# Kernel tuning notes

Measured on AMD Instinct MI355X. Metric: run time of the kernel, lower is better.

Reference implementation:

```python
import jax, jax.numpy as jnp
import numpy as np

EPS = 1e-5
V = 16  # num_nodes

def _bn(x, g, b, axes, ch):
    # training-mode BatchNorm (biased variance), channel axis = ch
    m = x.mean(axes, keepdims=True)
    v = x.var(axes, keepdims=True)
    sh = [1] * x.ndim
    sh[ch] = x.shape[ch]
    return (x - m) * jax.lax.rsqrt(v + EPS) * g.reshape(sh) + b.reshape(sh)

def _adp(nv1, nv2, max_num_neigh=1):
    # softmax(relu(nv1 @ nv2), dim=1), then keep entries > max(1/V, (k+1)-th largest) with straight-through mask
    A = jax.nn.softmax(jax.nn.relu(nv1 @ nv2), axis=1)
    kth = -jnp.sort(-A, axis=1)[:, max_num_neigh:max_num_neigh + 1]  # (k+1)-th largest per row == -kthvalue(-A, k+1)
    mask = ((A > 1.0 / A.shape[0]) & (A > kth)).astype(A.dtype)
    binm = jax.lax.stop_gradient(mask - A) + A  # straight-through estimator
    return A * binm

def _stgcn(x, A, gw, gb, b1g, b1b, tw, tb, b2g, b2b):
    # standard ST-GCN block with spatial kernel K=1, stride 1, identity residual (in==out)
    # x: (N,C,T,V)
    res = x
    y = jnp.einsum('oc,nctv->notv', gw, x) + gb[None, :, None, None]  # 1x1 conv
    y = jnp.einsum('nctv,vw->nctw', y, A)                              # graph aggregation
    y = jax.nn.relu(_bn(y, b1g, b1b, (0, 2, 3), 1))
    y = jax.lax.conv_general_dilated(y, tw[:, :, :, None], (1, 1), [(1, 1), (0, 0)],
                                     dimension_numbers=('NCHW', 'OIHW', 'NCHW'))  # temporal conv (kt,1)
    y = _bn(y + tb[None, :, None, None], b2g, b2b, (0, 2, 3), 1)
    return jax.nn.relu(y + res)

def _static(x, pw, pg, pb, tw, tg, tb):
    # x: (p,n,c,s)
    p, n, c, s = x.shape
    # p-branch: Conv1d(c->c, k=1, no bias) over node dim + BN1d (stats over n*s batch and length p)
    y = jnp.einsum('oc,pncs->nsop', pw, x)          # (n,s,c,p)
    y = _bn(y, pg, pb, (0, 1, 3), 2)
    # t-branch: grouped Conv1d over time, groups = p nodes, kernel 3, pad 1
    z = y.transpose(0, 3, 2, 1).reshape(n, p * c, s)
    z = jax.lax.conv_general_dilated(z, tw, (1,), [(1, 1)],
                                     dimension_numbers=('NCH', 'OIH', 'NCH'),
                                     feature_group_count=p)
    z = _bn(z, tg, tb, (0, 2), 1)
    return z.reshape(n, p, c, s).transpose(1, 0, 2, 3)  # (p,n,c,s)

def _forward(x, nv1, nv2,
             d1gw, d1gb, d1b1g, d1b1b, d1tw, d1tb, d1b2g, d1b2b,
             d2gw, d2gb, d2b1g, d2b1b, d2tw, d2tb, d2b2g, d2b2b,
             s1pw, s1pg, s1pb, s1tw, s1tg, s1tb,
             s2pw, s2pg, s2pb, s2tw, s2tg, s2tb):
    A = _adp(nv1, nv2, 1)
    d = _stgcn(x, A, d1gw, d1gb, d1b1g, d1b1b, d1tw, d1tb, d1b2g, d1b2b)
    d = _stgcn(d, A, d2gw, d2gb, d2b1g, d2b1b, d2tw, d2tb, d2b2g, d2b2b)
    d = d.max(axis=2)                      # (N,C,V) max over time
    xs = x.transpose(3, 0, 1, 2)           # (V,N,C,T)
    s = _static(xs, s1pw, s1pg, s1pb, s1tw, s1tg, s1tb)
    s = _static(s, s2pw, s2pg, s2pb, s2tw, s2tg, s2tb)
    s = s.transpose(1, 2, 3, 0).max(axis=2)  # (N,C,V)
    return jnp.concatenate([d, s], axis=2)   # (N,C,2V)

def setup_inputs():
    key = jax.random.key(0)
    N, C, T, kt = 32, 128, 256, 3
    ks = jax.random.split(key, 8)
    def nrm(k, sh, s=0.05):
        return jax.random.normal(k, sh, jnp.float32) * s
    inp = {'x': nrm(ks[0], (N, C, T, V), 1.0),
           'nv1': nrm(ks[1], (V, 64), 1.0),
           'nv2': nrm(ks[2], (64, V), 1.0)}
    def stgcn_p(k, pre):
        k1, k2 = jax.random.split(k)
        return {pre + 'gw': nrm(k1, (C, C)), pre + 'gb': jnp.zeros(C),
                pre + 'b1g': jnp.ones(C), pre + 'b1b': jnp.zeros(C),
                pre + 'tw': nrm(k2, (C, C, kt)), pre + 'tb': jnp.zeros(C),
                pre + 'b2g': jnp.ones(C), pre + 'b2b': jnp.zeros(C)}
    def static_p(k, pre):
        k1, k2 = jax.random.split(k)
        return {pre + 'pw': nrm(k1, (C, C)), pre + 'pg': jnp.ones(C), pre + 'pb': jnp.zeros(C),
                pre + 'tw': nrm(k2, (V * C, C, kt)), pre + 'tg': jnp.ones(V * C), pre + 'tb': jnp.zeros(V * C)}
    inp.update(stgcn_p(ks[3], 'd1'))
    inp.update(stgcn_p(ks[4], 'd2'))
    inp.update(static_p(ks[5], 's1'))
    inp.update(static_p(ks[6], 's2'))
    return inp

def reference(x, nv1, nv2,
              d1gw, d1gb, d1b1g, d1b1b, d1tw, d1tb, d1b2g, d1b2b,
              d2gw, d2gb, d2b1g, d2b1b, d2tw, d2tb, d2b2g, d2b2b,
              s1pw, s1pg, s1pb, s1tw, s1tg, s1tb,
              s2pw, s2pg, s2pb, s2tw, s2tg, s2tb):
    return _forward(x, nv1, nv2,
                    d1gw, d1gb, d1b1g, d1b1b, d1tw, d1tb, d1b2g, d1b2b,
                    d2gw, d2gb, d2b1g, d2b1b, d2tw, d2tb, d2b2g, d2b2b,
                    s1pw, s1pg, s1pb, s1tw, s1tg, s1tb,
                    s2pw, s2pg, s2pb, s2tw, s2tg, s2tb)
```

## Files before the change

### kernel.cpp

```cpp
#include <hip/hip_runtime.h>

#define EPSBN 1e-5f

typedef __attribute__((ext_vector_type(8))) __bf16 bf16x8;
typedef __attribute__((ext_vector_type(4))) float f32x4;
typedef __attribute__((ext_vector_type(8))) unsigned short us8;

__device__ inline unsigned short f2bf(float f) {
  unsigned u = __float_as_uint(f);
  u = (u + 0x7fffu + ((u >> 16) & 1u)) >> 16;
  return (unsigned short)u;
}
__device__ inline float bf2f(unsigned short h) {
  return __uint_as_float(((unsigned)h) << 16);
}

__global__ void k_adj(const float* __restrict__ nv1, const float* __restrict__ nv2,
                      float* __restrict__ A, float* __restrict__ sA,
                      int* __restrict__ cntA, int* __restrict__ lvA, float* __restrict__ lvalA) {
  __shared__ float M[16][16];
  int tid = threadIdx.x;
  int i = tid >> 4, j = tid & 15;
  float acc = 0.f;
  #pragma unroll
  for (int k = 0; k < 64; ++k) acc += nv1[i*64+k] * nv2[k*16+j];
  M[i][j] = fmaxf(acc, 0.f);
  __syncthreads();
  if (tid < 16) {
    float m = -1e30f;
    for (int c = 0; c < 16; ++c) m = fmaxf(m, M[tid][c]);
    float e[16]; float s = 0.f;
    for (int c = 0; c < 16; ++c) { e[c] = expf(M[tid][c] - m); s += e[c]; }
    float inv = 1.f / s;
    float t1 = -1e30f, t2 = -1e30f;
    for (int c = 0; c < 16; ++c) {
      float a = e[c] * inv; e[c] = a;
      if (a > t1) { t2 = t1; t1 = a; }
      else if (a > t2) t2 = a;
    }
    for (int c = 0; c < 16; ++c) {
      bool keep = (e[c] > (1.0f/16.0f)) && (e[c] > t2);
      M[tid][c] = keep ? e[c] : 0.f;
    }
  }
  __syncthreads();
  A[tid] = M[tid>>4][tid&15];
  if (tid < 16) {
    float s = 0.f;
    int cnt = 0;
    for (int v = 0; v < 16; ++v) {
      float a = M[v][tid];
      s += a;
      if (a != 0.f) { lvA[tid*16 + cnt] = v; lvalA[tid*16 + cnt] = a; ++cnt; }
    }
    sA[tid] = s;
    cntA[tid] = cnt;
  }
}

__global__ __launch_bounds__(256) void k_cvt_cw(const float* __restrict__ w,
                                                unsigned short* __restrict__ o) {
  int idx = blockIdx.x*256 + threadIdx.x;
  if (idx < 16384) o[idx] = f2bf(w[idx]);
}
__global__ __launch_bounds__(256) void k_cvt_tw(const float* __restrict__ w,
                                                unsigned short* __restrict__ o, int nOut) {
  int idx = blockIdx.x*256 + threadIdx.x;
  if (idx >= nOut*384) return;
  int oo = idx / 384;
  int r = idx - oo*384;
  int tap = r >> 7, c = r & 127;
  o[idx] = f2bf(w[(oo*128 + c)*3 + tap]);
}

__global__ __launch_bounds__(256) void k_xS(const float* __restrict__ x,
                                            unsigned short* __restrict__ xS) {
  __shared__ float tl[64*128];
  int b = blockIdx.x; int n = b >> 6; int t0q = b & 63;
  int tid = threadIdx.x;
  const float* xb = x + (long)n*524288 + t0q*64;
  for (int idx = tid; idx < 2048; idx += 256) {
    int c = idx >> 4, q = idx & 15;
    float4 v = *(const float4*)(xb + (long)c*4096 + q*4);
    int cb = c >> 2, cl = c & 3;
    #pragma unroll
    for (int j = 0; j < 4; ++j)
      tl[(4*q+j)*128 + (((cb ^ q) & 31) << 2) + cl] = ((const float*)&v)[j];
  }
  __syncthreads();
  for (int idx = tid; idx < 2048; idx += 256) {
    int pos = idx >> 5, cblk = idx & 31;
    f32x4 v = *(const f32x4*)&tl[pos*128 + (((cblk ^ (pos >> 2)) & 31) << 2)];
    ushort4 pk;
    pk.x = f2bf(v.x); pk.y = f2bf(v.y); pk.z = f2bf(v.z); pk.w = f2bf(v.w);
    int vv = pos & 15, tt = pos >> 4;
    *(ushort4*)(xS + ((long)(n*16+vv)*256 + t0q*4 + tt)*128 + cblk*4) = pk;
  }
}

__global__ __launch_bounds__(256) void k_aggGconv(
    const float* __restrict__ x,
    const int* __restrict__ cntA, const int* __restrict__ lvA, const float* __restrict__ lvalA,
    const unsigned short* __restrict__ Wb,
    unsigned short* __restrict__ out,
    const float* __restrict__ gb, const float* __restrict__ sAv,
    float* __restrict__ part)
{
  __shared__ float tl[64*128];
  __shared__ __align__(16) unsigned short Th[64*128];
  __shared__ int cntS[16];
  __shared__ int lvS[256];
  __shared__ float lvalS[256];
  int b = blockIdx.x; int n = b >> 6; int off = (b & 63) << 6;
  int tid = threadIdx.x;
  if (tid < 16) cntS[tid] = cntA[tid];
  lvS[tid] = lvA[tid];
  lvalS[tid] = lvalA[tid];
  const float* xb = x + (long)n*524288 + off;
  for (int idx = tid; idx < 2048; idx += 256) {
    int c = idx >> 4, q = idx & 15;
    float4 v = *(const float4*)(xb + (long)c*4096 + q*4);
    int cb = c >> 2, cl = c & 3;
    #pragma unroll
    for (int j = 0; j < 4; ++j)
      tl[(4*q+j)*128 + (((cb ^ q) & 31) << 2) + cl] = ((const float*)&v)[j];
  }
  __syncthreads();
  for (int idx = tid; idx < 1024; idx += 256) {
    int pos = idx >> 4, c8 = (idx & 15) << 3;
    int tt = pos >> 4, w = pos & 15;
    int cb0 = c8 >> 2, cb1 = cb0 + 1;
    f32x4 s0 = {0.f,0.f,0.f,0.f}, s1 = {0.f,0.f,0.f,0.f};
    int cw = cntS[w];
    for (int j = 0; j < cw; ++j) {
      int p = tt*16 + lvS[w*16 + j];
      float a = lvalS[w*16 + j];
      int sw = p >> 2;
      f32x4 x0 = *(const f32x4*)&tl[p*128 + (((cb0 ^ sw) & 31) << 2)];
      f32x4 x1 = *(const f32x4*)&tl[p*128 + (((cb1 ^ sw) & 31) << 2)];
      s0.x += a*x0.x; s0.y += a*x0.y; s0.z += a*x0.z; s0.w += a*x0.w;
      s1.x += a*x1.x; s1.y += a*x1.y; s1.z += a*x1.z; s1.w += a*x1.w;
    }
    us8 pk;
    pk[0]=f2bf(s0.x); pk[1]=f2bf(s0.y); pk[2]=f2bf(s0.z); pk[3]=f2bf(s0.w);
    pk[4]=f2bf(s1.x); pk[5]=f2bf(s1.y); pk[6]=f2bf(s1.z); pk[7]=f2bf(s1.w);
    int byteoff = (pos << 8) + (c8 << 1);
    byteoff ^= ((pos & 7) << 4);
    *(us8*)((char*)Th + byteoff) = pk;
  }
  __syncthreads();
  int wv = tid >> 6, lane = tid & 63, l15 = lane & 15, lhi = lane >> 4;
  int o0 = wv << 5;
  f32x4 zz = {0.f,0.f,0.f,0.f};
  f32x4 acc[2][4];
  #pragma unroll
  for (int i = 0; i < 2; ++i)
    #pragma unroll
    for (int q = 0; q < 4; ++q) acc[i][q] = zz;
  const unsigned short* wr0 = Wb + (long)(o0 + l15)*128 + lhi*8;
  const unsigned short* wr1 = wr0 + 16*128;
  #pragma unroll
  for (int kk = 0; kk < 4; ++kk) {
    int kc = kk*32 + lhi*8;
    bf16x8 a0 = *(const bf16x8*)(wr0 + kk*32);
    bf16x8 a1 = *(const bf16x8*)(wr1 + kk*32);
    #pragma unroll
    for (int pf = 0; pf < 4; ++pf) {
      int row = pf*16 + l15;
      int byteoff = (row << 8) + (kc << 1);
      byteoff ^= ((row & 7) << 4);
      bf16x8 bh = *(const bf16x8*)((const char*)Th + byteoff);
      acc[0][pf] = __builtin_amdgcn_mfma_f32_16x16x32_bf16(a0, bh, acc[0][pf], 0, 0, 0);
      acc[1][pf] = __builtin_amdgcn_mfma_f32_16x16x32_bf16(a1, bh, acc[1][pf], 0, 0, 0);
    }
  }
  float s1a[2][4], s2a[2][4];
  #pragma unroll
  for (int i = 0; i < 2; ++i)
    #pragma unroll
    for (int j = 0; j < 4; ++j) { s1a[i][j] = 0.f; s2a[i][j] = 0.f; }
  unsigned short* og = out + ((long)n*4096 + off)*128;
  #pragma unroll
  for (int of = 0; of < 2; ++of) {
    int oc = o0 + of*16 + lhi*4;
    #pragma unroll
    for (int pf = 0; pf < 4; ++pf) {
      int pos = pf*16 + l15;
      f32x4 r = acc[of][pf];
      float s = sAv[l15];
      r.x += gb[oc+0]*s; r.y += gb[oc+1]*s;
      r.z += gb[oc+2]*s; r.w += gb[oc+3]*s;
      ushort4 pk;
      pk.x = f2bf(r.x); pk.y = f2bf(r.y); pk.z = f2bf(r.z); pk.w = f2bf(r.w);
      *(ushort4*)(og + (long)pos*128 + oc) = pk;
      #pragma unroll
      for (int j = 0; j < 4; ++j) { s1a[of][j] += r[j]; s2a[of][j] += r[j]*r[j]; }
    }
  }
  #pragma unroll
  for (int of = 0; of < 2; ++of)
    #pragma unroll
    for (int j = 0; j < 4; ++j) {
      float a = s1a[of][j], b2 = s2a[of][j];
      #pragma unroll
      for (int m = 1; m < 16; m <<= 1) { a += __shfl_xor(a, m); b2 += __shfl_xor(b2, m); }
      s1a[of][j] = a; s2a[of][j] = b2;
    }
  float* red = tl;
  if (l15 == 0) {
    #pragma unroll
    for (int of = 0; of < 2; ++of)
      #pragma unroll
      for (int j = 0; j < 4; ++j) {
        int ch = o0 + of*16 + lhi*4 + j;
        red[ch] = s1a[of][j];
        red[128 + ch] = s2a[of][j];
      }
  }
  __syncthreads();
  part[(long)blockIdx.x*256 + tid] = red[tid];
}

__global__ __launch_bounds__(256) void k_combineAggGconv(
    const unsigned short* __restrict__ z, const float* __restrict__ x,
    const int* __restrict__ cntA, const int* __restrict__ lvA, const float* __restrict__ lvalA,
    const float* __restrict__ sc, const float* __restrict__ sh,
    const unsigned short* __restrict__ Wb,
    unsigned short* __restrict__ r2, unsigned short* __restrict__ out,
    const float* __restrict__ gb, const float* __restrict__ sAv,
    float* __restrict__ part)
{
  __shared__ float rl[64*128];
  __shared__ __align__(16) unsigned short Th[64*128];
  __shared__ int cntS[16];
  __shared__ int lvS[256];
  __shared__ float lvalS[256];
  int b = blockIdx.x; int n = b >> 6; int off = (b & 63) << 6;
  int tid = threadIdx.x;
  if (tid < 16) cntS[tid] = cntA[tid];
  lvS[tid] = lvA[tid];
  lvalS[tid] = lvalA[tid];
  long zbase = (long)b * 8192;
  for (int idx = tid; idx < 1024; idx += 256) {
    int pos = idx >> 4, c8 = (idx & 15) << 3;
    us8 raw = *(const us8*)(z + zbase + (long)pos*128 + c8);
    int qp = pos >> 2;
    #pragma unroll
    for (int half = 0; half < 2; ++half) {
      f32x4 f;
      #pragma unroll
      for (int j = 0; j < 4; ++j) {
        int cc = c8 + half*4 + j;
        f[j] = bf2f(raw[half*4+j]) * sc[cc] + sh[cc];
      }
      int cblk = (c8 >> 2) + half;
      *(f32x4*)&rl[pos*128 + (((cblk ^ qp) & 31) << 2)] = f;
    }
  }
  __syncthreads();
  const float* xb = x + (long)n*524288 + off;
  for (int idx = tid; idx < 2048; idx += 256) {
    int c = idx >> 4, q = idx & 15;
    float4 v = *(const float4*)(xb + (long)c*4096 + q*4);
    int cb = c >> 2, cl = c & 3;
    #pragma unroll
    for (int j = 0; j < 4; ++j) {
      int a = (4*q+j)*128 + (((cb ^ q) & 31) << 2) + cl;
      rl[a] = fmaxf(rl[a] + ((const float*)&v)[j], 0.f);
    }
  }
  __syncthreads();
  for (int idx = tid; idx < 1024; idx += 256) {
    int pos = idx >> 4, c8 = (idx & 15) << 3;
    int cb0 = c8 >> 2, cb1 = cb0 + 1;
    int qp = pos >> 2;
    f32x4 r0 = *(const f32x4*)&rl[pos*128 + (((cb0 ^ qp) & 31) << 2)];
    f32x4 r1 = *(const f32x4*)&rl[pos*128 + (((cb1 ^ qp) & 31) << 2)];
    us8 pr;
    pr[0]=f2bf(r0.x); pr[1]=f2bf(r0.y); pr[2]=f2bf(r0.z); pr[3]=f2bf(r0.w);
    pr[4]=f2bf(r1.x); pr[5]=f2bf(r1.y); pr[6]=f2bf(r1.z); pr[7]=f2bf(r1.w);
    *(us8*)(r2 + zbase + (long)pos*128 + c8) = pr;
    int tt = pos >> 4, w = pos & 15;
    f32x4 s0 = {0.f,0.f,0.f,0.f}, s1 = {0.f,0.f,0.f,0.f};
    int cw = cntS[w];
    for (int j = 0; j < cw; ++j) {
      int p = tt*16 + lvS[w*16 + j];
      float a = lvalS[w*16 + j];
      int sw = p >> 2;
      f32x4 x0 = *(const f32x4*)&rl[p*128 + (((cb0 ^ sw) & 31) << 2)];
      f32x4 x1 = *(const f32x4*)&rl[p*128 + (((cb1 ^ sw) & 31) << 2)];
      s0.x += a*x0.x; s0.y += a*x0.y; s0.z += a*x0.z; s0.w += a*x0.w;
      s1.x += a*x1.x; s1.y += a*x1.y; s1.z += a*x1.z; s1.w += a*x1.w;
    }
    us8 pk;
    pk[0]=f2bf(s0.x); pk[1]=f2bf(s0.y); pk[2]=f2bf(s0.z); pk[3]=f2bf(s0.w);
    pk[4]=f2bf(s1.x); pk[5]=f2bf(s1.y); pk[6]=f2bf(s1.z); pk[7]=f2bf(s1.w);
    int byteoff = (pos << 8) + (c8 << 1);
    byteoff ^= ((pos & 7) << 4);
    *(us8*)((char*)Th + byteoff) = pk;
  }
  __syncthreads();
  int wv = tid >> 6, lane = tid & 63, l15 = lane & 15, lhi = lane >> 4;
  int o0 = wv << 5;
  f32x4 zz = {0.f,0.f,0.f,0.f};
  f32x4 acc[2][4];
  #pragma unroll
  for (int i = 0; i < 2; ++i)
    #pragma unroll
    for (int q = 0; q < 4; ++q) acc[i][q] = zz;
  const unsigned short* wr0 = Wb + (long)(o0 + l15)*128 + lhi*8;
  const unsigned short* wr1 = wr0 + 16*128;
  #pragma unroll
  for (int kk = 0; kk < 4; ++kk) {
    int kc = kk*32 + lhi*8;
    bf16x8 a0 = *(const bf16x8*)(wr0 + kk*32);
    bf16x8 a1 = *(const bf16x8*)(wr1 + kk*32);
    #pragma unroll
    for (int pf = 0; pf < 4; ++pf) {
      int row = pf*16 + l15;
      int byteoff = (row << 8) + (kc << 1);
      byteoff ^= ((row & 7) << 4);
      bf16x8 bh = *(const bf16x8*)((const char*)Th + byteoff);
      acc[0][pf] = __builtin_amdgcn_mfma_f32_16x16x32_bf16(a0, bh, acc[0][pf], 0, 0, 0);
      acc[1][pf] = __builtin_amdgcn_mfma_f32_16x16x32_bf16(a1, bh, acc[1][pf], 0, 0, 0);
    }
  }
  float s1a[2][4], s2a[2][4];
  #pragma unroll
  for (int i = 0; i < 2; ++i)
    #pragma unroll
    for (int j = 0; j < 4; ++j) { s1a[i][j] = 0.f; s2a[i][j] = 0.f; }
  unsigned short* og = out + zbase;
  #pragma unroll
  for (int of = 0; of < 2; ++of) {
    int oc = o0 + of*16 + lhi*4;
    #pragma unroll
    for (int pf = 0; pf < 4; ++pf) {
      int pos = pf*16 + l15;
      f32x4 r = acc[of][pf];
      float s = sAv[l15];
      r.x += gb[oc+0]*s; r.y += gb[oc+1]*s;
      r.z += gb[oc+2]*s; r.w += gb[oc+3]*s;
      ushort4 pk;
      pk.x = f2bf(r.x); pk.y = f2bf(r.y); pk.z = f2bf(r.z); pk.w = f2bf(r.w);
      *(ushort4*)(og + (long)pos*128 + oc) = pk;
      #pragma unroll
      for (int j = 0; j < 4; ++j) { s1a[of][j] += r[j]; s2a[of][j] += r[j]*r[j]; }
    }
  }
  #pragma unroll
  for (int of = 0; of < 2; ++of)
    #pragma unroll
    for (int j = 0; j < 4; ++j) {
      float a = s1a[of][j], b2 = s2a[of][j];
      #pragma unroll
      for (int m = 1; m < 16; m <<= 1) { a += __shfl_xor(a, m); b2 += __shfl_xor(b2, m); }
      s1a[of][j] = a; s2a[of][j] = b2;
    }
  float* red = rl;
  __syncthreads();
  if (l15 == 0) {
    #pragma unroll
    for (int of = 0; of < 2; ++of)
      #pragma unroll
      for (int j = 0; j < 4; ++j) {
        int ch = o0 + of*16 + lhi*4 + j;
        red[ch] = s1a[of][j];
        red[128 + ch] = s2a[of][j];
      }
  }
  __syncthreads();
  part[(long)blockIdx.x*256 + tid] = red[tid];
}

template<int POSB, int HALO, int TAPS, int GROUPED_W, int IN_BN, int GROUPED_BN, int RELU_IN>
__global__ __launch_bounds__(256) void k_conv(
    const unsigned short* __restrict__ in, const unsigned short* __restrict__ Wb,
    unsigned short* __restrict__ out, int L,
    const float* __restrict__ isc, const float* __restrict__ ish,
    float* __restrict__ part)
{
  constexpr int TW = POSB + 2*HALO;
  constexpr int PF = POSB / 16;
  constexpr int KT = TAPS*128;
  __shared__ __align__(16) unsigned short Th[TW*128];
  int tid = threadIdx.x;
  int bpg = L / POSB;
  int g = blockIdx.x / bpg;
  int pos0 = (blockIdx.x - g*bpg) * POSB;
  const unsigned short* ing = in + (long)g*L*128;

  int cbase = (IN_BN && GROUPED_BN) ? ((g & 15) << 7) : 0;
  for (int idx = tid; idx < TW*16; idx += 256) {
    int row = idx >> 4;
    int c8 = (idx & 15) << 3;
    int gp = pos0 + row - HALO;
    us8 h = (us8)0;
    if (gp >= 0 && gp < L) {
      us8 raw = *(const us8*)(ing + (long)gp*128 + c8);
      if (IN_BN) {
        #pragma unroll
        for (int j = 0; j < 8; ++j) {
          int ci = cbase + c8 + j;
          float v = bf2f(raw[j]) * isc[ci] + ish[ci];
          if (RELU_IN) v = fmaxf(v, 0.f);
          h[j] = f2bf(v);
        }
      } else {
        h = raw;
      }
    }
    int byteoff = (row << 8) + (c8 << 1);
    byteoff ^= ((row & 7) << 4);
    *(us8*)((char*)Th + byteoff) = h;
  }
  __syncthreads();

  int wv = tid >> 6, lane = tid & 63, l15 = lane & 15, lhi = lane >> 4;
  int o0 = wv << 5;

  f32x4 zz = {0.f,0.f,0.f,0.f};
  f32x4 acc[2][PF];
  #pragma unroll
  for (int i = 0; i < 2; ++i)
    #pragma unroll
    for (int q = 0; q < PF; ++q) acc[i][q] = zz;

  const unsigned short* Wg = Wb + (GROUPED_W ? (long)(g & 15)*128*KT : 0);
  const unsigned short* wr0 = Wg + (long)(o0 + l15)*KT + lhi*8;
  const unsigned short* wr1 = wr0 + 16*KT;

  #pragma unroll
  for (int tap = 0; tap < TAPS; ++tap) {
    #pragma unroll
    for (int kk = 0; kk < 4; ++kk) {
      int kc = kk*32 + lhi*8;
      bf16x8 a0 = *(const bf16x8*)(wr0 + tap*128 + kk*32);
      bf16x8 a1 = *(const bf16x8*)(wr1 + tap*128 + kk*32);
      #pragma unroll
      for (int pf = 0; pf < PF; ++pf) {
        int row = pf*16 + l15 + tap*HALO;
        int byteoff = (row << 8) + (kc << 1);
        byteoff ^= ((row & 7) << 4);
        bf16x8 bh = *(const bf16x8*)((const char*)Th + byteoff);
        acc[0][pf] = __builtin_amdgcn_mfma_f32_16x16x32_bf16(a0, bh, acc[0][pf], 0, 0, 0);
        acc[1][pf] = __builtin_amdgcn_mfma_f32_16x16x32_bf16(a1, bh, acc[1][pf], 0, 0, 0);
      }
    }
  }

  float s1a[2][4], s2a[2][4];
  #pragma unroll
  for (int i = 0; i < 2; ++i)
    #pragma unroll
    for (int j = 0; j < 4; ++j) { s1a[i][j] = 0.f; s2a[i][j] = 0.f; }

  unsigned short* og = out + ((long)g*L + pos0)*128;
  #pragma unroll
  for (int of = 0; of < 2; ++of) {
    int oc = o0 + of*16 + lhi*4;
    #pragma unroll
    for (int pf = 0; pf < PF; ++pf) {
      int pos = pf*16 + l15;
      f32x4 r = acc[of][pf];
      ushort4 pk;
      pk.x = f2bf(r.x); pk.y = f2bf(r.y); pk.z = f2bf(r.z); pk.w = f2bf(r.w);
      *(ushort4*)(og + (long)pos*128 + oc) = pk;
      #pragma unroll
      for (int j = 0; j < 4; ++j) { s1a[of][j] += r[j]; s2a[of][j] += r[j]*r[j]; }
    }
  }
  #pragma unroll
  for (int of = 0; of < 2; ++of)
    #pragma unroll
    for (int j = 0; j < 4; ++j) {
      float a = s1a[of][j], b2 = s2a[of][j];
      #pragma unroll
      for (int m = 1; m < 16; m <<= 1) { a += __shfl_xor(a, m); b2 += __shfl_xor(b2, m); }
      s1a[of][j] = a; s2a[of][j] = b2;
    }
  __syncthreads();
  float* red = (float*)Th;
  if (l15 == 0) {
    #pragma unroll
    for (int of = 0; of < 2; ++of)
      #pragma unroll
      for (int j = 0; j < 4; ++j) {
        int ch = o0 + of*16 + lhi*4 + j;
        red[ch] = s1a[of][j];
        red[128 + ch] = s2a[of][j];
      }
  }
  __syncthreads();
  part[(long)blockIdx.x*256 + tid] = red[tid];
}

__global__ __launch_bounds__(256) void k_bnfin128(const float* __restrict__ part,
                           const float* __restrict__ gamma, const float* __restrict__ beta,
                           float* __restrict__ sc, float* __restrict__ sh,
                           float invN, int nblk) {
  int c = blockIdx.x, tid = threadIdx.x;
  float s1 = 0.f, s2 = 0.f;
  for (int b = tid; b < nblk; b += 256) {
    s1 += part[b*256 + c];
    s2 += part[b*256 + 128 + c];
  }
  __shared__ float l1[256], l2[256];
  l1[tid] = s1; l2[tid] = s2;
  __syncthreads();
  for (int st = 128; st > 0; st >>= 1) {
    if (tid < st) { l1[tid] += l1[tid+st]; l2[tid] += l2[tid+st]; }
    __syncthreads();
  }
  if (tid == 0) {
    float mean = l1[0]*invN;
    float var  = l2[0]*invN - mean*mean;
    float s = gamma[c] * rsqrtf(var + EPSBN);
    sc[c] = s;
    sh[c] = beta[c] - mean*s;
  }
}

__global__ void k_bnfin2048(const float* __restrict__ part,
                            const float* __restrict__ gamma, const float* __restrict__ beta,
                            float* __restrict__ sc, float* __restrict__ sh, float invN) {
  int ch = blockIdx.x; int v = ch >> 7, c = ch & 127;
  int lane = threadIdx.x;
  int n = lane >> 1, bp = lane & 1;
  int blk = ((n*16 + v) << 1) + bp;
  float s1 = part[blk*256 + c];
  float s2 = part[blk*256 + 128 + c];
  for (int m = 32; m > 0; m >>= 1) { s1 += __shfl_down(s1, m); s2 += __shfl_down(s2, m); }
  if (lane == 0) {
    float mean = s1*invN;
    float var  = s2*invN - mean*mean;
    float s = gamma[ch] * rsqrtf(var + EPSBN);
    sc[ch] = s;
    sh[ch] = beta[ch] - mean*s;
  }
}

__global__ __launch_bounds__(256) void k_maxdyn(
    const unsigned short* __restrict__ z, const unsigned short* __restrict__ res,
    const float* __restrict__ sc, const float* __restrict__ sh,
    float* __restrict__ outp)
{
  int b = blockIdx.x; int n = b >> 4, v = b & 15;
  int tid = threadIdx.x; int c = tid & 127, h = tid >> 7;
  const unsigned short* zb = z   + ((long)n*4096 + v)*128 + c;
  const unsigned short* rb = res + ((long)n*4096 + v)*128 + c;
  float s = sc[c], bb = sh[c];
  float m = 0.f;
  for (int t = h; t < 256; t += 2) {
    float val = bf2f(zb[(long)t*2048]) * s + bb + bf2f(rb[(long)t*2048]);
    m = fmaxf(m, val);
  }
  __shared__ float red[256];
  red[tid] = m;
  __syncthreads();
  if (tid < 128)
    outp[(long)n*4096 + c*32 + v] = fmaxf(fmaxf(red[tid], red[tid+128]), 0.f);
}

__global__ __launch_bounds__(256) void k_maxstat(
    const unsigned short* __restrict__ z,
    const float* __restrict__ sc, const float* __restrict__ sh,
    float* __restrict__ outp)
{
  int b = blockIdx.x; int n = b >> 4, v = b & 15;
  int tid = threadIdx.x; int c = tid & 127, h = tid >> 7;
  const unsigned short* zb = z + (long)b*256*128 + c;
  float s = sc[v*128 + c], bb = sh[v*128 + c];
  float m = -1e30f;
  for (int t = h; t < 256; t += 2)
    m = fmaxf(m, bf2f(zb[t*128]) * s + bb);
  __shared__ float red[256];
  red[tid] = m;
  __syncthreads();
  if (tid < 128)
    outp[(long)n*4096 + c*32 + 16 + v] = fmaxf(red[tid], red[tid+128]);
}

extern "C" void kernel_launch(void* const* d_in, const int* in_sizes, int n_in,
                              void* d_out, int out_size, void* d_ws, size_t ws_size,
                              hipStream_t stream) {
  (void)in_sizes; (void)n_in; (void)out_size; (void)ws_size;
  const float* x     = (const float*)d_in[0];
  const float* nv1   = (const float*)d_in[1];
  const float* nv2   = (const float*)d_in[2];
  const float* d1gw  = (const float*)d_in[3];
  const float* d1gb  = (const float*)d_in[4];
  const float* d1b1g = (const float*)d_in[5];
  const float* d1b1b = (const float*)d_in[6];
  const float* d1tw  = (const float*)d_in[7];
  const float* d1b2g = (const float*)d_in[9];
  const float* d1b2b = (const float*)d_in[10];
  const float* d2gw  = (const float*)d_in[11];
  const float* d2gb  = (const float*)d_in[12];
  const float* d2b1g = (const float*)d_in[13];
  const float* d2b1b = (const float*)d_in[14];
  const float* d2tw  = (const float*)d_in[15];
  const float* d2b2g = (const float*)d_in[17];
  const float* d2b2b = (const float*)d_in[18];
  const float* s1pw  = (const float*)d_in[19];
  const float* s1pg  = (const float*)d_in[20];
  const float* s1pb  = (const float*)d_in[21];
  const float* s1tw  = (const float*)d_in[22];
  const float* s1tg  = (const float*)d_in[23];
  const float* s1tb  = (const float*)d_in[24];
  const float* s2pw  = (const float*)d_in[25];
  const float* s2pg  = (const float*)d_in[26];
  const float* s2pb  = (const float*)d_in[27];
  const float* s2tw  = (const float*)d_in[28];
  const float* s2tg  = (const float*)d_in[29];
  const float* s2tb  = (const float*)d_in[30];

  float* W = (float*)d_ws;
  float* Am  = W;
  float* sAv = W + 256;
  float* scA = W + 512;  float* shA = W + 640;
  float* scB = W + 768;  float* shB = W + 896;
  float* scC = W + 1024; float* shC = W + 1152;
  float* scD = W + 1280; float* shD = W + 1408;
  float* scE = W + 1536; float* shE = W + 1664;
  float* scG = W + 1792; float* shG = W + 1920;
  float* scF = W + 2048; float* shF = W + 4096;
  float* scH = W + 6144; float* shH = W + 8192;
  int*   cntA  = (int*)(W + 10240);
  int*   lvA   = (int*)(W + 10496);
  float* lvalA = W + 10752;
  float* A = W + 16384;
  float* B = A + 16777216;
  float* C = B + 16777216;
  float* part = C + 16777216;
  float* outp = (float*)d_out;

  unsigned short* A0 = (unsigned short*)A;
  unsigned short* B0 = (unsigned short*)B;
  unsigned short* C0 = (unsigned short*)C;
  unsigned short* w_d1g = (unsigned short*)(A + 8388608);
  unsigned short* w_d1t = w_d1g + 16384;
  unsigned short* w_d2g = w_d1t + 49152;
  unsigned short* w_d2t = w_d2g + 16384;
  unsigned short* w_s1p = (unsigned short*)(C + 8388608);
  unsigned short* w_s1t = (unsigned short*)(B + 8388608);
  unsigned short* w_s2p = w_s1t + 786432;
  unsigned short* w_s2t = w_s2p + 16384;

  k_adj<<<1, 256, 0, stream>>>(nv1, nv2, Am, sAv, cntA, lvA, lvalA);
  k_cvt_cw<<<64, 256, 0, stream>>>(d1gw, w_d1g);
  k_cvt_tw<<<192, 256, 0, stream>>>(d1tw, w_d1t, 128);
  k_cvt_cw<<<64, 256, 0, stream>>>(d2gw, w_d2g);
  k_cvt_tw<<<192, 256, 0, stream>>>(d2tw, w_d2t, 128);
  k_cvt_cw<<<64, 256, 0, stream>>>(s1pw, w_s1p);
  k_cvt_tw<<<3072, 256, 0, stream>>>(s1tw, w_s1t, 2048);
  k_cvt_cw<<<64, 256, 0, stream>>>(s2pw, w_s2p);
  k_cvt_tw<<<3072, 256, 0, stream>>>(s2tw, w_s2t, 2048);

  k_aggGconv<<<2048, 256, 0, stream>>>(x, cntA, lvA, lvalA, w_d1g, B0, d1gb, sAv, part);
  k_bnfin128<<<128, 256, 0, stream>>>(part, d1b1g, d1b1b, scA, shA, 1.f/131072.f, 2048);
  k_conv<128,16,3,0,1,0,1><<<1024, 256, 0, stream>>>(B0, w_d1t, C0, 4096, scA, shA, part);
  k_bnfin128<<<128, 256, 0, stream>>>(part, d1b2g, d1b2b, scB, shB, 1.f/131072.f, 1024);
  k_combineAggGconv<<<2048, 256, 0, stream>>>(C0, x, cntA, lvA, lvalA, scB, shB, w_d2g, A0, B0, d2gb, sAv, part);
  k_bnfin128<<<128, 256, 0, stream>>>(part, d2b1g, d2b1b, scC, shC, 1.f/131072.f, 2048);
  k_conv<128,16,3,0,1,0,1><<<1024, 256, 0, stream>>>(B0, w_d2t, C0, 4096, scC, shC, part);
  k_bnfin128<<<128, 256, 0, stream>>>(part, d2b2g, d2b2b, scD, shD, 1.f/131072.f, 1024);
  k_maxdyn<<<512, 256, 0, stream>>>(C0, A0, scD, shD, outp);

  k_xS<<<2048, 256, 0, stream>>>(x, B0);
  k_conv<128,0,1,0,0,0,0><<<1024, 256, 0, stream>>>(B0, w_s1p, A0, 256, nullptr, nullptr, part);
  k_bnfin128<<<128, 256, 0, stream>>>(part, s1pg, s1pb, scE, shE, 1.f/131072.f, 1024);
  k_conv<128,1,3,1,1,0,0><<<1024, 256, 0, stream>>>(A0, w_s1t, C0, 256, scE, shE, part);
  k_bnfin2048<<<2048, 64, 0, stream>>>(part, s1tg, s1tb, scF, shF, 1.f/8192.f);
  k_conv<128,0,1,0,1,1,0><<<1024, 256, 0, stream>>>(C0, w_s2p, A0, 256, scF, shF, part);
  k_bnfin128<<<128, 256, 0, stream>>>(part, s2pg, s2pb, scG, shG, 1.f/131072.f, 1024);
  k_conv<128,1,3,1,1,0,0><<<1024, 256, 0, stream>>>(A0, w_s2t, C0, 256, scG, shG, part);
  k_bnfin2048<<<2048, 64, 0, stream>>>(part, s2tg, s2tb, scH, shH, 1.f/8192.f);
  k_maxstat<<<512, 256, 0, stream>>>(C0, scH, shH, outp);
}
```

Before: 372.3 us.

## Convert input to bf16 once and share it across dynamic and static branches

Adds a single transpose-and-convert kernel that writes x as bf16 in two layouts, position-major for the dynamic branch and node-major for the static branch. The aggregation-gconv and combine kernels now read this bf16 copy instead of transposing fp32 x through shared memory each time, and the combine kernel keeps the residual in bf16 shared memory. The eight weight-conversion launches are merged into two kernels, and buffers are reassigned, with the dynamic weights placed in the output buffer. The aim is to cut global traffic, LDS use and launch count. In exchange, the residual x now enters in bf16, which lowers precision, and the buffer aliasing has to stay correct.

```diff
diff --git a/kernel.cpp b/kernel.cpp
--- a/kernel.cpp
+++ b/kernel.cpp
@@ -58,23 +58,39 @@
   }
 }
 
-__global__ __launch_bounds__(256) void k_cvt_cw(const float* __restrict__ w,
-                                                unsigned short* __restrict__ o) {
-  int idx = blockIdx.x*256 + threadIdx.x;
-  if (idx < 16384) o[idx] = f2bf(w[idx]);
-}
-__global__ __launch_bounds__(256) void k_cvt_tw(const float* __restrict__ w,
-                                                unsigned short* __restrict__ o, int nOut) {
-  int idx = blockIdx.x*256 + threadIdx.x;
-  if (idx >= nOut*384) return;
-  int oo = idx / 384;
-  int r = idx - oo*384;
+__device__ inline void cvt_cw_seg(const float* w, unsigned short* o, int lidx) {
+  o[lidx] = f2bf(w[lidx]);
+}
+__device__ inline void cvt_tw_seg(const float* w, unsigned short* o, int lidx) {
+  int oo = lidx / 384;
+  int r = lidx - oo*384;
   int tap = r >> 7, c = r & 127;
-  o[idx] = f2bf(w[(oo*128 + c)*3 + tap]);
-}
-
-__global__ __launch_bounds__(256) void k_xS(const float* __restrict__ x,
-                                            unsigned short* __restrict__ xS) {
+  o[lidx] = f2bf(w[(oo*128 + c)*3 + tap]);
+}
+__global__ __launch_bounds__(256) void k_cvt_dyn(
+    const float* __restrict__ d1g, const float* __restrict__ d1t,
+    const float* __restrict__ d2g, const float* __restrict__ d2t,
+    unsigned short* __restrict__ O) {
+  int b = blockIdx.x, tid = threadIdx.x;
+  if (b < 64)        cvt_cw_seg(d1g, O,          b*256 + tid);
+  else if (b < 256)  cvt_tw_seg(d1t, O + 16384, (b-64)*256 + tid);
+  else if (b < 320)  cvt_cw_seg(d2g, O + 65536, (b-256)*256 + tid);
+  else               cvt_tw_seg(d2t, O + 81920, (b-320)*256 + tid);
+}
+__global__ __launch_bounds__(256) void k_cvt_stat(
+    const float* __restrict__ s1p, const float* __restrict__ s1t,
+    const float* __restrict__ s2p, const float* __restrict__ s2t,
+    unsigned short* __restrict__ S) {
+  int b = blockIdx.x, tid = threadIdx.x;
+  if (b < 64)        cvt_cw_seg(s1p, S,           b*256 + tid);
+  else if (b < 3136) cvt_tw_seg(s1t, S + 16384,  (b-64)*256 + tid);
+  else if (b < 3200) cvt_cw_seg(s2p, S + 802816, (b-3136)*256 + tid);
+  else               cvt_tw_seg(s2t, S + 819200, (b-3200)*256 + tid);
+}
+
+__global__ __launch_bounds__(256) void k_xcvt(const float* __restrict__ x,
+                                              unsigned short* __restrict__ xB,
+                                              unsigned short* __restrict__ xS) {
   __shared__ float tl[64*128];
   int b = blockIdx.x; int n = b >> 6; int t0q = b & 63;
   int tid = threadIdx.x;
@@ -88,25 +104,28 @@
       tl[(4*q+j)*128 + (((cb ^ q) & 31) << 2) + cl] = ((const float*)&v)[j];
   }
   __syncthreads();
-  for (int idx = tid; idx < 2048; idx += 256) {
-    int pos = idx >> 5, cblk = idx & 31;
-    f32x4 v = *(const f32x4*)&tl[pos*128 + (((cblk ^ (pos >> 2)) & 31) << 2)];
-    ushort4 pk;
-    pk.x = f2bf(v.x); pk.y = f2bf(v.y); pk.z = f2bf(v.z); pk.w = f2bf(v.w);
+  for (int idx = tid; idx < 1024; idx += 256) {
+    int pos = idx >> 4, c8 = (idx & 15) << 3;
+    int cb0 = c8 >> 2, cb1 = cb0 + 1, qp = pos >> 2;
+    f32x4 v0 = *(const f32x4*)&tl[pos*128 + (((cb0 ^ qp) & 31) << 2)];
+    f32x4 v1 = *(const f32x4*)&tl[pos*128 + (((cb1 ^ qp) & 31) << 2)];
+    us8 pk;
+    pk[0]=f2bf(v0.x); pk[1]=f2bf(v0.y); pk[2]=f2bf(v0.z); pk[3]=f2bf(v0.w);
+    pk[4]=f2bf(v1.x); pk[5]=f2bf(v1.y); pk[6]=f2bf(v1.z); pk[7]=f2bf(v1.w);
+    *(us8*)(xB + ((long)n*4096 + t0q*64 + pos)*128 + c8) = pk;
     int vv = pos & 15, tt = pos >> 4;
-    *(ushort4*)(xS + ((long)(n*16+vv)*256 + t0q*4 + tt)*128 + cblk*4) = pk;
+    *(us8*)(xS + ((long)(n*16+vv)*256 + t0q*4 + tt)*128 + c8) = pk;
   }
 }
 
 __global__ __launch_bounds__(256) void k_aggGconv(
-    const float* __restrict__ x,
+    const unsigned short* __restrict__ xB,
     const int* __restrict__ cntA, const int* __restrict__ lvA, const float* __restrict__ lvalA,
     const unsigned short* __restrict__ Wb,
     unsigned short* __restrict__ out,
     const float* __restrict__ gb, const float* __restrict__ sAv,
     float* __restrict__ part)
 {
-  __shared__ float tl[64*128];
   __shared__ __align__(16) unsigned short Th[64*128];
   __shared__ int cntS[16];
   __shared__ int lvS[256];
@@ -116,34 +135,25 @@
   if (tid < 16) cntS[tid] = cntA[tid];
   lvS[tid] = lvA[tid];
   lvalS[tid] = lvalA[tid];
-  const float* xb = x + (long)n*524288 + off;
-  for (int idx = tid; idx < 2048; idx += 256) {
-    int c = idx >> 4, q = idx & 15;
-    float4 v = *(const float4*)(xb + (long)c*4096 + q*4);
-    int cb = c >> 2, cl = c & 3;
-    #pragma unroll
-    for (int j = 0; j < 4; ++j)
-      tl[(4*q+j)*128 + (((cb ^ q) & 31) << 2) + cl] = ((const float*)&v)[j];
-  }
-  __syncthreads();
+  __syncthreads();
+  const unsigned short* xbase = xB + ((long)n*4096 + off)*128;
   for (int idx = tid; idx < 1024; idx += 256) {
     int pos = idx >> 4, c8 = (idx & 15) << 3;
     int tt = pos >> 4, w = pos & 15;
-    int cb0 = c8 >> 2, cb1 = cb0 + 1;
-    f32x4 s0 = {0.f,0.f,0.f,0.f}, s1 = {0.f,0.f,0.f,0.f};
+    float s[8];
+    #pragma unroll
+    for (int k = 0; k < 8; ++k) s[k] = 0.f;
     int cw = cntS[w];
     for (int j = 0; j < cw; ++j) {
       int p = tt*16 + lvS[w*16 + j];
       float a = lvalS[w*16 + j];
-      int sw = p >> 2;
-      f32x4 x0 = *(const f32x4*)&tl[p*128 + (((cb0 ^ sw) & 31) << 2)];
-      f32x4 x1 = *(const f32x4*)&tl[p*128 + (((cb1 ^ sw) & 31) << 2)];
-      s0.x += a*x0.x; s0.y += a*x0.y; s0.z += a*x0.z; s0.w += a*x0.w;
-      s1.x += a*x1.x; s1.y += a*x1.y; s1.z += a*x1.z; s1.w += a*x1.w;
+      us8 raw = *(const us8*)(xbase + (long)p*128 + c8);
+      #pragma unroll
+      for (int k = 0; k < 8; ++k) s[k] += a * bf2f(raw[k]);
     }
     us8 pk;
-    pk[0]=f2bf(s0.x); pk[1]=f2bf(s0.y); pk[2]=f2bf(s0.z); pk[3]=f2bf(s0.w);
-    pk[4]=f2bf(s1.x); pk[5]=f2bf(s1.y); pk[6]=f2bf(s1.z); pk[7]=f2bf(s1.w);
+    #pragma unroll
+    for (int k = 0; k < 8; ++k) pk[k] = f2bf(s[k]);
     int byteoff = (pos << 8) + (c8 << 1);
     byteoff ^= ((pos & 7) << 4);
     *(us8*)((char*)Th + byteoff) = pk;
@@ -206,7 +216,8 @@
       for (int m = 1; m < 16; m <<= 1) { a += __shfl_xor(a, m); b2 += __shfl_xor(b2, m); }
       s1a[of][j] = a; s2a[of][j] = b2;
     }
-  float* red = tl;
+  __syncthreads();
+  float* red = (float*)Th;
   if (l15 == 0) {
     #pragma unroll
     for (int of = 0; of < 2; ++of)
@@ -222,7 +233,7 @@
 }
 
 __global__ __launch_bounds__(256) void k_combineAggGconv(
-    const unsigned short* __restrict__ z, const float* __restrict__ x,
+    const unsigned short* __restrict__ z, const unsigned short* __restrict__ xB,
     const int* __restrict__ cntA, const int* __restrict__ lvA, const float* __restrict__ lvalA,
     const float* __restrict__ sc, const float* __restrict__ sh,
     const unsigned short* __restrict__ Wb,
@@ -230,12 +241,12 @@
     const float* __restrict__ gb, const float* __restrict__ sAv,
     float* __restrict__ part)
 {
-  __shared__ float rl[64*128];
+  __shared__ __align__(16) unsigned short rl[64*128];
   __shared__ __align__(16) unsigned short Th[64*128];
   __shared__ int cntS[16];
   __shared__ int lvS[256];
   __shared__ float lvalS[256];
-  int b = blockIdx.x; int n = b >> 6; int off = (b & 63) << 6;
+  int b = blockIdx.x;
   int tid = threadIdx.x;
   if (tid < 16) cntS[tid] = cntA[tid];
   lvS[tid] = lvA[tid];
@@ -243,58 +254,36 @@
   long zbase = (long)b * 8192;
   for (int idx = tid; idx < 1024; idx += 256) {
     int pos = idx >> 4, c8 = (idx & 15) << 3;
-    us8 raw = *(const us8*)(z + zbase + (long)pos*128 + c8);
-    int qp = pos >> 2;
-    #pragma unroll
-    for (int half = 0; half < 2; ++half) {
-      f32x4 f;
-      #pragma unroll
-      for (int j = 0; j < 4; ++j) {
-        int cc = c8 + half*4 + j;
-        f[j] = bf2f(raw[half*4+j]) * sc[cc] + sh[cc];
-      }
-      int cblk = (c8 >> 2) + half;
-      *(f32x4*)&rl[pos*128 + (((cblk ^ qp) & 31) << 2)] = f;
-    }
-  }
-  __syncthreads();
-  const float* xb = x + (long)n*524288 + off;
-  for (int idx = tid; idx < 2048; idx += 256) {
-    int c = idx >> 4, q = idx & 15;
-    float4 v = *(const float4*)(xb + (long)c*4096 + q*4);
-    int cb = c >> 2, cl = c & 3;
-    #pragma unroll
-    for (int j = 0; j < 4; ++j) {
-      int a = (4*q+j)*128 + (((cb ^ q) & 31) << 2) + cl;
-      rl[a] = fmaxf(rl[a] + ((const float*)&v)[j], 0.f);
-    }
+    us8 zr = *(const us8*)(z  + zbase + (long)pos*128 + c8);
+    us8 xr = *(const us8*)(xB + zbase + (long)pos*128 + c8);
+    us8 pr;
+    #pragma unroll
+    for (int k = 0; k < 8; ++k) {
+      int cc = c8 + k;
+      float v = bf2f(zr[k]) * sc[cc] + sh[cc] + bf2f(xr[k]);
+      pr[k] = f2bf(fmaxf(v, 0.f));
+    }
+    *(us8*)(rl + pos*128 + c8) = pr;
+    *(us8*)(r2 + zbase + (long)pos*128 + c8) = pr;
   }
   __syncthreads();
   for (int idx = tid; idx < 1024; idx += 256) {
     int pos = idx >> 4, c8 = (idx & 15) << 3;
-    int cb0 = c8 >> 2, cb1 = cb0 + 1;
-    int qp = pos >> 2;
-    f32x4 r0 = *(const f32x4*)&rl[pos*128 + (((cb0 ^ qp) & 31) << 2)];
-    f32x4 r1 = *(const f32x4*)&rl[pos*128 + (((cb1 ^ qp) & 31) << 2)];
-    us8 pr;
-    pr[0]=f2bf(r0.x); pr[1]=f2bf(r0.y); pr[2]=f2bf(r0.z); pr[3]=f2bf(r0.w);
-    pr[4]=f2bf(r1.x); pr[5]=f2bf(r1.y); pr[6]=f2bf(r1.z); pr[7]=f2bf(r1.w);
-    *(us8*)(r2 + zbase + (long)pos*128 + c8) = pr;
     int tt = pos >> 4, w = pos & 15;
-    f32x4 s0 = {0.f,0.f,0.f,0.f}, s1 = {0.f,0.f,0.f,0.f};
+    float s[8];
+    #pragma unroll
+    for (int k = 0; k < 8; ++k) s[k] = 0.f;
     int cw = cntS[w];
     for (int j = 0; j < cw; ++j) {
       int p = tt*16 + lvS[w*16 + j];
       float a = lvalS[w*16 + j];
-      int sw = p >> 2;
-      f32x4 x0 = *(const f32x4*)&rl[p*128 + (((cb0 ^ sw) & 31) << 2)];
-      f32x4 x1 = *(const f32x4*)&rl[p*128 + (((cb1 ^ sw) & 31) << 2)];
-      s0.x += a*x0.x; s0.y += a*x0.y; s0.z += a*x0.z; s0.w += a*x0.w;
-      s1.x += a*x1.x; s1.y += a*x1.y; s1.z += a*x1.z; s1.w += a*x1.w;
+      us8 raw = *(const us8*)(rl + p*128 + c8);
+      #pragma unroll
+      for (int k = 0; k < 8; ++k) s[k] += a * bf2f(raw[k]);
     }
     us8 pk;
-    pk[0]=f2bf(s0.x); pk[1]=f2bf(s0.y); pk[2]=f2bf(s0.z); pk[3]=f2bf(s0.w);
-    pk[4]=f2bf(s1.x); pk[5]=f2bf(s1.y); pk[6]=f2bf(s1.z); pk[7]=f2bf(s1.w);
+    #pragma unroll
+    for (int k = 0; k < 8; ++k) pk[k] = f2bf(s[k]);
     int byteoff = (pos << 8) + (c8 << 1);
     byteoff ^= ((pos & 7) << 4);
     *(us8*)((char*)Th + byteoff) = pk;
@@ -357,8 +346,8 @@
       for (int m = 1; m < 16; m <<= 1) { a += __shfl_xor(a, m); b2 += __shfl_xor(b2, m); }
       s1a[of][j] = a; s2a[of][j] = b2;
     }
-  float* red = rl;
-  __syncthreads();
+  __syncthreads();
+  float* red = (float*)rl;
   if (l15 == 0) {
     #pragma unroll
     for (int of = 0; of < 2; ++of)
@@ -636,45 +625,46 @@
   float* outp = (float*)d_out;
 
   unsigned short* A0 = (unsigned short*)A;
+  unsigned short* A1 = (unsigned short*)(A + 8388608);
   unsigned short* B0 = (unsigned short*)B;
+  unsigned short* B1 = (unsigned short*)(B + 8388608);
   unsigned short* C0 = (unsigned short*)C;
-  unsigned short* w_d1g = (unsigned short*)(A + 8388608);
-  unsigned short* w_d1t = w_d1g + 16384;
-  unsigned short* w_d2g = w_d1t + 49152;
-  unsigned short* w_d2t = w_d2g + 16384;
-  unsigned short* w_s1p = (unsigned short*)(C + 8388608);
-  unsigned short* w_s1t = (unsigned short*)(B + 8388608);
-  unsigned short* w_s2p = w_s1t + 786432;
-  unsigned short* w_s2t = w_s2p + 16384;
+  unsigned short* C1 = (unsigned short*)(C + 8388608);
+
+  unsigned short* OW = (unsigned short*)d_out;
+  unsigned short* w_d1g = OW;
+  unsigned short* w_d1t = OW + 16384;
+  unsigned short* w_d2g = OW + 65536;
+  unsigned short* w_d2t = OW + 81920;
+  unsigned short* SW    = B1;
+  unsigned short* w_s1p = SW;
+  unsigned short* w_s1t = SW + 16384;
+  unsigned short* w_s2p = SW + 802816;
+  unsigned short* w_s2t = SW + 819200;
 
   k_adj<<<1, 256, 0, stream>>>(nv1, nv2, Am, sAv, cntA, lvA, lvalA);
-  k_cvt_cw<<<64, 256, 0, stream>>>(d1gw, w_d1g);
-  k_cvt_tw<<<192, 256, 0, stream>>>(d1tw, w_d1t, 128);
-  k_cvt_cw<<<64, 256, 0, stream>>>(d2gw, w_d2g);
-  k_cvt_tw<<<192, 256, 0, stream>>>(d2tw, w_d2t, 128);
-  k_cvt_cw<<<64, 256, 0, stream>>>(s1pw, w_s1p);
-  k_cvt_tw<<<3072, 256, 0, stream>>>(s1tw, w_s1t, 2048);
-  k_cvt_cw<<<64, 256, 0, stream>>>(s2pw, w_s2p);
-  k_cvt_tw<<<3072, 256, 0, stream>>>(s2tw, w_s2t, 2048);
-
-  k_aggGconv<<<2048, 256, 0, stream>>>(x, cntA, lvA, lvalA, w_d1g, B0, d1gb, sAv, part);
+  k_cvt_dyn<<<512, 256, 0, stream>>>(d1gw, d1tw, d2gw, d2tw, OW);
+  k_xcvt<<<2048, 256, 0, stream>>>(x, A0, A1);
+
+  k_aggGconv<<<2048, 256, 0, stream>>>(A0, cntA, lvA, lvalA, w_d1g, B0, d1gb, sAv, part);
   k_bnfin128<<<128, 256, 0, stream>>>(part, d1b1g, d1b1b, scA, shA, 1.f/131072.f, 2048);
   k_conv<128,16,3,0,1,0,1><<<1024, 256, 0, stream>>>(B0, w_d1t, C0, 4096, scA, shA, part);
   k_bnfin128<<<128, 256, 0, stream>>>(part, d1b2g, d1b2b, scB, shB, 1.f/131072.f, 1024);
-  k_combineAggGconv<<<2048, 256, 0, stream>>>(C0, x, cntA, lvA, lvalA, scB, shB, w_d2g, A0, B0, d2gb, sAv, part);
+  k_combineAggGconv<<<2048, 256, 0, stream>>>(C0, A0, cntA, lvA, lvalA, scB, shB, w_d2g,
+                                              B0, C1, d2gb, sAv, part);
   k_bnfin128<<<128, 256, 0, stream>>>(part, d2b1g, d2b1b, scC, shC, 1.f/131072.f, 2048);
-  k_conv<128,16,3,0,1,0,1><<<1024, 256, 0, stream>>>(B0, w_d2t, C0, 4096, scC, shC, part);
+  k_conv<128,16,3,0,1,0,1><<<1024, 256, 0, stream>>>(C1, w_d2t, B1, 4096, scC, shC, part);
   k_bnfin128<<<128, 256, 0, stream>>>(part, d2b2g, d2b2b, scD, shD, 1.f/131072.f, 1024);
-  k_maxdyn<<<512, 256, 0, stream>>>(C0, A0, scD, shD, outp);
-
-  k_xS<<<2048, 256, 0, stream>>>(x, B0);
-  k_conv<128,0,1,0,0,0,0><<<1024, 256, 0, stream>>>(B0, w_s1p, A0, 256, nullptr, nullptr, part);
+  k_maxdyn<<<512, 256, 0, stream>>>(B1, B0, scD, shD, outp);
+
+  k_cvt_stat<<<6272, 256, 0, stream>>>(s1pw, s1tw, s2pw, s2tw, SW);
+  k_conv<128,0,1,0,0,0,0><<<1024, 256, 0, stream>>>(A1, w_s1p, C0, 256, nullptr, nullptr, part);
   k_bnfin128<<<128, 256, 0, stream>>>(part, s1pg, s1pb, scE, shE, 1.f/131072.f, 1024);
-  k_conv<128,1,3,1,1,0,0><<<1024, 256, 0, stream>>>(A0, w_s1t, C0, 256, scE, shE, part);
+  k_conv<128,1,3,1,1,0,0><<<1024, 256, 0, stream>>>(C0, w_s1t, A0, 256, scE, shE, part);
   k_bnfin2048<<<2048, 64, 0, stream>>>(part, s1tg, s1tb, scF, shF, 1.f/8192.f);
-  k_conv<128,0,1,0,1,1,0><<<1024, 256, 0, stream>>>(C0, w_s2p, A0, 256, scF, shF, part);
+  k_conv<128,0,1,0,1,1,0><<<1024, 256, 0, stream>>>(A0, w_s2p, C0, 256, scF, shF, part);
   k_bnfin128<<<128, 256, 0, stream>>>(part, s2pg, s2pb, scG, shG, 1.f/131072.f, 1024);
-  k_conv<128,1,3,1,1,0,0><<<1024, 256, 0, stream>>>(A0, w_s2t, C0, 256, scG, shG, part);
+  k_conv<128,1,3,1,1,0,0><<<1024, 256, 0, stream>>>(C0, w_s2t, A0, 256, scG, shG, part);
   k_bnfin2048<<<2048, 64, 0, stream>>>(part, s2tg, s2tb, scH, shH, 1.f/8192.f);
-  k_maxstat<<<512, 256, 0, stream>>>(C0, scH, shH, outp);
-}
+  k_maxstat<<<512, 256, 0, stream>>>(A0, scH, shH, outp);
+}
```

Result: faster. 361.0 us (-3.0%).
